# Kernel tuning notes

Hardware: AMD Instinct MI355X
Metric: run time of the kernel (lower is better)

## Reference

```python
import jax, jax.numpy as jnp
import numpy as np

B, S, H, E, R, V, NC = 256, 100, 512, 512, 50, 50000, 5


def setup_inputs() -> dict:
    key = jax.random.key(0)
    ks = jax.random.split(key, 16)
    g = lambda k, shp, s=0.05: jax.random.normal(k, shp, dtype=jnp.float32) * s
    return dict(
        sentence=jax.random.randint(ks[0], (B, S), 0, V),
        decoder_state=g(ks[1], (B, H), 1.0),
        encoder_outputs=g(ks[2], (B, S, H), 1.0),
        word_emb=g(ks[3], (V, E)),
        rel_emb=g(ks[4], (R + 1, E)),
        sos_emb=g(ks[5], (1, E)),
        W_comb=g(ks[6], (E, H + E)), b_comb=jnp.zeros((E,), jnp.float32),
        W_attn=g(ks[7], (1, 2 * H)), b_attn=jnp.zeros((1,), jnp.float32),
        W_ih=g(ks[8], (NC, 3 * H, E)), W_hh=g(ks[9], (NC, 3 * H, H)),
        b_ih=jnp.zeros((NC, 3 * H), jnp.float32), b_hh=jnp.zeros((NC, 3 * H), jnp.float32),
        W_eos=g(ks[10], (1, H)), b_eos=jnp.zeros((1,), jnp.float32),
        W_pred=g(ks[11], (R, H)), b_pred=jnp.zeros((R,), jnp.float32),
        W_fuse=g(ks[12], (100, 2 * H)), b_fuse=jnp.zeros((100,), jnp.float32),
        W_copy=g(ks[13], (1, 100)), b_copy=jnpp.zeros((1,), jnp.float32) if False else jnp.zeros((1,), jnp.float32),
    )


def _gru_step(x, h, Wih, Whh, bih, bhh):
    # torch GRU gate order: r, z, n
    gi = x @ Wih.T + bih          # [B, 3H]
    gh = h @ Whh.T + bhh          # [B, 3H]
    ir, iz, inn = jnp.split(gi, 3, axis=-1)
    hr, hz, hn = jnp.split(gh, 3, axis=-1)
    r = jax.nn.sigmoid(ir + hr)
    z = jax.nn.sigmoid(iz + hz)
    n = jnp.tanh(inn + r * hn)
    return (1.0 - z) * n + z * h


def _decode_step(emb, h, enc, cell, p):
    # attention: softmax over sequence dim of a 1-dim score
    h_exp = jnp.broadcast_to(h[:, None, :], enc.shape)          # [B, S, H]
    scores = jnp.concatenate([h_exp, enc], axis=-1) @ p['W_attn'].T + p['b_attn']  # [B,S,1]
    aw = jax.nn.softmax(scores, axis=1)
    context = jnp.sum(aw * enc, axis=1)                          # [B, H]
    x = jnp.concatenate([emb, context], axis=-1) @ p['W_comb'].T + p['b_comb']     # [B, E]
    h_new = _gru_step(x, h, p['W_ih'][cell], p['W_hh'][cell], p['b_ih'][cell], p['b_hh'][cell])
    out = h_new                                                  # GRU output == new state
    eos = out @ p['W_eos'].T + p['b_eos']                        # [B, 1]
    pred = jax.nn.log_softmax(jnp.concatenate([out @ p['W_pred'].T + p['b_pred'], eos], axis=-1), axis=-1)  # [B, R+1]
    fused = jax.nn.selu(jnp.concatenate([jnp.broadcast_to(out[:, None, :], enc.shape), enc], axis=-1))       # [B,S,2H]
    fused = jax.nn.selu(fused @ p['W_fuse'].T + p['b_fuse'])     # [B, S, 100]
    copy = (fused @ p['W_copy'].T + p['b_copy'])[..., 0]        # [B, S]
    copy = jax.nn.log_softmax(jnp.concatenate([copy, eos], axis=-1), axis=-1)  # [B, S+1]
    return pred, copy, h_new


def _forward(sentence, decoder_state, encoder_outputs, word_emb, rel_emb, sos_emb, p):
    b = sentence.shape[0]
    s = sentence.shape[1]
    output = jnp.broadcast_to(sos_emb[0], (b, sos_emb.shape[1]))  # SOS embedding
    enc_state = decoder_state
    prev_state = jnp.zeros_like(decoder_state)
    n_cells = p['W_ih'].shape[0]
    rel_logits, copy_logits, actions = [], [], []
    for c in range(n_cells):
        h = (enc_state + prev_state) * 0.5
        for t in range(3):
            pred, copy, h = _decode_step(output, h, encoder_outputs, c, p)
            if t == 0:
                act = jnp.argmax(pred, axis=1)                   # [B] in [0, R]
                rel_logits.append(pred)
                output = rel_emb[act]
            else:
                act = jnp.argmax(copy, axis=1)                   # [B] in [0, S]
                copy_logits.append(copy)
                word = jnp.take_along_axis(sentence, jnp.clip(act, 0, s - 1)[:, None], axis=1)[:, 0]
                output = word_emb[word]
            actions.append(act)
        prev_state = h
    return jnp.stack(rel_logits), jnp.stack(copy_logits), jnp.stack(actions)


def reference(sentence, decoder_state, encoder_outputs, word_emb, rel_emb, sos_emb,
              W_comb, b_comb, W_attn, b_attn, W_ih, W_hh, b_ih, b_hh,
              W_eos, b_eos, W_pred, b_pred, W_fuse, b_fuse, W_copy, b_copy):
    p = dict(W_comb=W_comb, b_comb=b_comb, W_attn=W_attn, b_attn=b_attn,
             W_ih=W_ih, W_hh=W_hh, b_ih=b_ih, b_hh=b_hh,
             W_eos=W_eos, b_eos=b_eos, W_pred=W_pred, b_pred=b_pred,
             W_fuse=W_fuse, b_fuse=b_fuse, W_copy=W_copy, b_copy=b_copy)
    return _forward(sentence, decoder_state, encoder_outputs, word_emb, rel_emb, sos_emb, p)
```

## Files before the change

kernel.cpp:

```cpp
#include <hip/hip_runtime.h>
#include <math.h>

#define B 256
#define S 100
#define H 512
#define E 512
#define R 50
#define NC 5
#define H3 1536

__device__ __forceinline__ float selu_f(float x){
    return x > 0.0f ? 1.0507009873554805f * x
                    : 1.7580993408473766f * expm1f(x);
}
__device__ __forceinline__ float wred_sum(float v){
    #pragma unroll
    for (int o = 32; o > 0; o >>= 1) v += __shfl_xor(v, o);
    return v;
}
__device__ __forceinline__ float wred_maxf(float v){
    #pragma unroll
    for (int o = 32; o > 0; o >>= 1) v = fmaxf(v, __shfl_xor(v, o));
    return v;
}

struct GSmem {
    alignas(16) float As[16][68];
    alignas(16) float Ws[16][132];
};

__device__ __forceinline__ void gemm64(
    GSmem& sm,
    const float* __restrict__ A, int lda, int M,
    const float* __restrict__ W, int ldw,
    const float* __restrict__ bias,
    const float* __restrict__ addm, int ldadd,
    float* __restrict__ C, int ldc,
    int N, int m0, int n0, int k0beg, int k0end, int seluA)
{
    const int t  = threadIdx.x;
    const int tx = t & 15;
    const int ty = t >> 4;
    const int lm = t >> 2,  lk  = (t & 3) << 2;
    const int lw = t >> 1,  lkw = (t & 1) << 3;
    int am = m0 + lm; if (am >= M) am = M - 1;
    const float* Ap = A + (size_t)am * lda + lk;
    const int nw = n0 + lw;
    const float* Wp = W + (size_t)nw * ldw + lkw;
    const bool wok = (nw < N);
    const float4 f40 = make_float4(0.f, 0.f, 0.f, 0.f);

    float4 ar = *(const float4*)(Ap + k0beg);
    if (seluA){ ar.x = selu_f(ar.x); ar.y = selu_f(ar.y); ar.z = selu_f(ar.z); ar.w = selu_f(ar.w); }
    float4 w0 = wok ? *(const float4*)(Wp + k0beg)     : f40;
    float4 w1 = wok ? *(const float4*)(Wp + k0beg + 4) : f40;

    float acc[4][8] = {};
    for (int k0 = k0beg; k0 < k0end; k0 += 16){
        if (k0 != k0beg) __syncthreads();
        sm.As[lk+0][lm] = ar.x; sm.As[lk+1][lm] = ar.y;
        sm.As[lk+2][lm] = ar.z; sm.As[lk+3][lm] = ar.w;
        sm.Ws[lkw+0][lw] = w0.x; sm.Ws[lkw+1][lw] = w0.y;
        sm.Ws[lkw+2][lw] = w0.z; sm.Ws[lkw+3][lw] = w0.w;
        sm.Ws[lkw+4][lw] = w1.x; sm.Ws[lkw+5][lw] = w1.y;
        sm.Ws[lkw+6][lw] = w1.z; sm.Ws[lkw+7][lw] = w1.w;
        __syncthreads();
        if (k0 + 16 < k0end){
            ar = *(const float4*)(Ap + k0 + 16);
            if (seluA){ ar.x = selu_f(ar.x); ar.y = selu_f(ar.y); ar.z = selu_f(ar.z); ar.w = selu_f(ar.w); }
            w0 = wok ? *(const float4*)(Wp + k0 + 16)     : f40;
            w1 = wok ? *(const float4*)(Wp + k0 + 16 + 4) : f40;
        }
        #pragma unroll
        for (int kk = 0; kk < 16; ++kk){
            const float4 av  = *(const float4*)&sm.As[kk][ty*4];
            const float4 wv0 = *(const float4*)&sm.Ws[kk][tx*4];
            const float4 wv1 = *(const float4*)&sm.Ws[kk][tx*4 + 64];
            const float aa[4] = {av.x, av.y, av.z, av.w};
            const float bb[8] = {wv0.x, wv0.y, wv0.z, wv0.w, wv1.x, wv1.y, wv1.z, wv1.w};
            #pragma unroll
            for (int i = 0; i < 4; ++i)
                #pragma unroll
                for (int j = 0; j < 8; ++j)
                    acc[i][j] += aa[i] * bb[j];
        }
    }
    #pragma unroll
    for (int i = 0; i < 4; ++i){
        const int m = m0 + ty*4 + i;
        if (m < M){
            #pragma unroll
            for (int j = 0; j < 8; ++j){
                const int n = n0 + ((j < 4) ? (tx*4 + j) : (64 + tx*4 + j - 4));
                if (n < N){
                    float vv = acc[i][j];
                    if (bias) vv += bias[n];
                    if (addm) vv += addm[(size_t)m * ldadd + n];
                    C[(size_t)m * ldc + n] = vv;
                }
            }
        }
    }
}

struct GS128 {
    alignas(16) float As[16][132];
    alignas(16) float Ws[16][132];
};

__device__ __forceinline__ void gemm128(
    GS128& sm,
    const float* __restrict__ A, int lda, int M,
    const float* __restrict__ W, int ldw,
    const float* __restrict__ bias,
    const float* __restrict__ addm, int ldadd,
    float* __restrict__ C, int ldc,
    int N, int m0, int n0, int K, int seluA)
{
    const int t  = threadIdx.x;
    const int tx = t & 15, ty = t >> 4;
    const int lr = t >> 1, lk = (t & 1) << 3;
    int am = m0 + lr; if (am >= M) am = M - 1;
    const float* Ap = A + (size_t)am * lda + lk;
    const int nw = n0 + lr;
    const float* Wp = W + (size_t)nw * ldw + lk;
    const bool wok = (nw < N);
    const float4 f40 = make_float4(0.f, 0.f, 0.f, 0.f);

    float4 a0 = *(const float4*)Ap;
    float4 a1 = *(const float4*)(Ap + 4);
    float4 w0 = wok ? *(const float4*)Wp       : f40;
    float4 w1 = wok ? *(const float4*)(Wp + 4) : f40;

    float acc[8][8] = {};
    for (int k0 = 0; k0 < K; k0 += 16){
        if (k0) __syncthreads();
        float4 sa0 = a0, sa1 = a1;
        if (seluA){
            sa0.x = selu_f(sa0.x); sa0.y = selu_f(sa0.y);
            sa0.z = selu_f(sa0.z); sa0.w = selu_f(sa0.w);
            sa1.x = selu_f(sa1.x); sa1.y = selu_f(sa1.y);
            sa1.z = selu_f(sa1.z); sa1.w = selu_f(sa1.w);
        }
        sm.As[lk+0][lr] = sa0.x; sm.As[lk+1][lr] = sa0.y;
        sm.As[lk+2][lr] = sa0.z; sm.As[lk+3][lr] = sa0.w;
        sm.As[lk+4][lr] = sa1.x; sm.As[lk+5][lr] = sa1.y;
        sm.As[lk+6][lr] = sa1.z; sm.As[lk+7][lr] = sa1.w;
        sm.Ws[lk+0][lr] = w0.x;  sm.Ws[lk+1][lr] = w0.y;
        sm.Ws[lk+2][lr] = w0.z;  sm.Ws[lk+3][lr] = w0.w;
        sm.Ws[lk+4][lr] = w1.x;  sm.Ws[lk+5][lr] = w1.y;
        sm.Ws[lk+6][lr] = w1.z;  sm.Ws[lk+7][lr] = w1.w;
        __syncthreads();
        if (k0 + 16 < K){
            a0 = *(const float4*)(Ap + k0 + 16);
            a1 = *(const float4*)(Ap + k0 + 20);
            w0 = wok ? *(const float4*)(Wp + k0 + 16) : f40;
            w1 = wok ? *(const float4*)(Wp + k0 + 20) : f40;
        }
        #pragma unroll
        for (int kk = 0; kk < 16; ++kk){
            const float4 av0 = *(const float4*)&sm.As[kk][ty*4];
            const float4 av1 = *(const float4*)&sm.As[kk][ty*4 + 64];
            const float4 wv0 = *(const float4*)&sm.Ws[kk][tx*4];
            const float4 wv1 = *(const float4*)&sm.Ws[kk][tx*4 + 64];
            const float aa[8] = {av0.x, av0.y, av0.z, av0.w, av1.x, av1.y, av1.z, av1.w};
            const float bb[8] = {wv0.x, wv0.y, wv0.z, wv0.w, wv1.x, wv1.y, wv1.z, wv1.w};
            #pragma unroll
            for (int i = 0; i < 8; ++i)
                #pragma unroll
                for (int j = 0; j < 8; ++j)
                    acc[i][j] += aa[i] * bb[j];
        }
    }
    #pragma unroll
    for (int i = 0; i < 8; ++i){
        const int m = m0 + ((i < 4) ? (ty*4 + i) : (64 + ty*4 + i - 4));
        if (m < M){
            #pragma unroll
            for (int j = 0; j < 8; ++j){
                const int n = n0 + ((j < 4) ? (tx*4 + j) : (64 + tx*4 + j - 4));
                if (n < N){
                    float vv = acc[i][j];
                    if (bias) vv += bias[n];
                    if (addm) vv += addm[(size_t)m * ldadd + n];
                    C[(size_t)m * ldc + n] = vv;
                }
            }
        }
    }
}

struct GemmJob {
    const float* A; int lda; long long sA; int M;
    const float* W; int ldw; long long sW;
    const float* bias; long long sBias;
    const float* addm; int ldadd; long long sAddm;
    float* C; int ldc; long long sC;
    int N, K, seluA;
    int nx, ny, base;
};
struct Jobs4 { GemmJob j[4]; };

__global__ __launch_bounds__(256) void k_mgemm(Jobs4 js)
{
    __shared__ GS128 sm;
    const int bid = blockIdx.x;
    GemmJob j;
    if      (bid >= js.j[3].base) j = js.j[3];
    else if (bid >= js.j[2].base) j = js.j[2];
    else if (bid >= js.j[1].base) j = js.j[1];
    else                          j = js.j[0];
    const int local = bid - j.base;
    const int z = local / (j.nx * j.ny);
    const int r = local % (j.nx * j.ny);
    const int y = r / j.nx, x = r % j.nx;
    gemm128(sm,
            j.A + (size_t)z * j.sA, j.lda, j.M,
            j.W + (size_t)z * j.sW, j.ldw,
            j.bias ? j.bias + (size_t)z * j.sBias : nullptr,
            j.addm ? j.addm + (size_t)z * j.sAddm : nullptr, j.ldadd,
            j.C + (size_t)z * j.sC, j.ldc,
            j.N, y * 128, x * 128, j.K, j.seluA);
}

__global__ __launch_bounds__(256) void k_pre0(
    const float* __restrict__ sos, const float* __restrict__ dec,
    const float* __restrict__ enc, const float* __restrict__ W_attn,
    const float* __restrict__ W_comb, const float* __restrict__ b_comb,
    const float* __restrict__ rel_emb, const float* __restrict__ W_fuse,
    float* __restrict__ emb, float* __restrict__ h0,
    float* __restrict__ WcT, float* __restrict__ xc,
    float* __restrict__ relx, float* __restrict__ v_buf)
{
    __shared__ __align__(16) char smraw[sizeof(GS128)];
    const int bid = blockIdx.x, t = threadIdx.x;
    if (bid < 8){
        for (int idx = bid * 256 + t; idx < B * E; idx += 8 * 256){
            emb[idx] = sos[idx & (E - 1)];
            h0[idx]  = 0.5f * dec[idx];
        }
    } else if (bid < 136){
        float (*tile)[65] = (float(*)[65])smraw;
        const int tt = bid - 8;
        const int bx = (tt & 15) * 64;
        const int by = (tt >> 4) * 64;
        const int c4 = (t & 15) * 4, rg = t >> 4;
        for (int rr = 0; rr < 64; rr += 16){
            float4 v = *(const float4*)(W_comb + (size_t)(by + rg + rr) * (H + E) + bx + c4);
            tile[rg + rr][c4+0] = v.x; tile[rg + rr][c4+1] = v.y;
            tile[rg + rr][c4+2] = v.z; tile[rg + rr][c4+3] = v.w;
        }
        __syncthreads();
        for (int rr = 0; rr < 64; rr += 16){
            WcT[(size_t)(bx + rg + rr) * E + by + c4 + 0] = tile[c4+0][rg + rr];
            WcT[(size_t)(bx + rg + rr) * E + by + c4 + 1] = tile[c4+1][rg + rr];
            WcT[(size_t)(bx + rg + rr) * E + by + c4 + 2] = tile[c4+2][rg + rr];
            WcT[(size_t)(bx + rg + rr) * E + by + c4 + 3] = tile[c4+3][rg + rr];
        }
    } else if (bid < 392){
        float* aw   = (float*)smraw;
        float* red  = aw + 128;
        float* ctxl = red + 128;
        const int b = bid - 136;
        const int wv = t >> 6, ln = t & 63;
        const float* eb = enc + (size_t)b * S * H;
        const float* wa = W_attn + H;
        for (int s = wv; s < S; s += 4){
            const float* es = eb + (size_t)s * H;
            float a = 0.f;
            #pragma unroll
            for (int u = 0; u < H/64; ++u) a += es[ln + 64*u] * wa[ln + 64*u];
            a = wred_sum(a);
            if (ln == 0) aw[s] = a;
        }
        __syncthreads();
        float vm = (t < S) ? aw[t] : -INFINITY;
        if (t < 128) red[t] = vm;
        __syncthreads();
        for (int st = 64; st > 0; st >>= 1){
            if (t < st) red[t] = fmaxf(red[t], red[t + st]);
            __syncthreads();
        }
        const float m = red[0];
        __syncthreads();
        float e = (t < S) ? expf(aw[t] - m) : 0.f;
        if (t < 128) red[t] = e;
        __syncthreads();
        for (int st = 64; st > 0; st >>= 1){
            if (t < st) red[t] += red[t + st];
            __syncthreads();
        }
        const float sum = red[0];
        __syncthreads();
        if (t < S) aw[t] = e / sum;
        __syncthreads();
        for (int hh = t; hh < H; hh += 256){
            float a = 0.f;
            for (int s = 0; s < S; ++s) a += aw[s] * eb[(size_t)s * H + hh];
            ctxl[hh] = a;
        }
        __syncthreads();
        for (int n = wv; n < E; n += 4){
            const float* wr = W_comb + (size_t)n * (H + E) + E;
            float a = 0.f;
            #pragma unroll
            for (int u = 0; u < H/64; ++u) a += ctxl[ln + 64*u] * wr[ln + 64*u];
            a = wred_sum(a);
            if (ln == 0) xc[(size_t)b * E + n] = a + b_comb[n];
        }
    } else if (bid < 396){
        GS128& sm = *(GS128*)smraw;
        gemm128(sm, rel_emb, E, R + 1, W_comb, H + E, nullptr, nullptr, 0,
                relx, E, E, 0, (bid - 392) * 128, E, 0);
    } else {
        GS128& sm = *(GS128*)smraw;
        gemm128(sm, enc, H, B * S, W_fuse + H, 2 * H, nullptr, nullptr, 0,
                v_buf, 100, 100, (bid - 396) * 128, 0, H, 1);
    }
}

struct GSmemK64 {
    alignas(16) float As[64][68];
    alignas(16) float Ws[64][132];
};

__global__ __launch_bounds__(256) void k_gru2_k64(
    const float* emb, const float* h,
    const float* Wihc, const float* Whh,
    const float* gixc, const float* bhh,
    float* gip, float* ghp, int giOn)
{
    __shared__ GSmemK64 sm;
    const int t = threadIdx.x;
    int xt = blockIdx.x;
    const int m0 = blockIdx.y * 64;
    const int z  = blockIdx.z;
    const int kb = z * 64;

    const float* A; int lda; const float* W; int ldw;
    const float* bias = nullptr; const float* addm = nullptr;
    float* C;
    if (giOn && xt < 12){
        A = emb; lda = E; W = Wihc; ldw = E;
        if (z == 0) addm = gixc;
        C = gip + (size_t)z * B * H3;
    } else {
        if (giOn) xt -= 12;
        A = h; lda = H; W = Whh; ldw = H;
        if (z == 0) bias = bhh;
        C = ghp + (size_t)z * B * H3;
    }
    const int n0 = xt * 128;

    {
        const int lm = t >> 2, ks = (t & 3) << 4;
        const float* Ap = A + (size_t)(m0 + lm) * lda + kb + ks;
        #pragma unroll
        for (int q = 0; q < 4; ++q){
            float4 a = *(const float4*)(Ap + 4*q);
            sm.As[ks + 4*q + 0][lm] = a.x;
            sm.As[ks + 4*q + 1][lm] = a.y;
            sm.As[ks + 4*q + 2][lm] = a.z;
            sm.As[ks + 4*q + 3][lm] = a.w;
        }
    }
    {
        const int lw = t >> 1, ks2 = (t & 1) << 5;
        const float* Wp = W + (size_t)(n0 + lw) * ldw + kb + ks2;
        #pragma unroll
        for (int q = 0; q < 8; ++q){
            float4 w = *(const float4*)(Wp + 4*q);
            sm.Ws[ks2 + 4*q + 0][lw] = w.x;
            sm.Ws[ks2 + 4*q + 1][lw] = w.y;
            sm.Ws[ks2 + 4*q + 2][lw] = w.z;
            sm.Ws[ks2 + 4*q + 3][lw] = w.w;
        }
    }
    __syncthreads();

    const int tx = t & 15, ty = t >> 4;
    float acc[4][8] = {};
    #pragma unroll 16
    for (int kk = 0; kk < 64; ++kk){
        const float4 av  = *(const float4*)&sm.As[kk][ty*4];
        const float4 wv0 = *(const float4*)&sm.Ws[kk][tx*4];
        const float4 wv1 = *(const float4*)&sm.Ws[kk][tx*4 + 64];
        const float aa[4] = {av.x, av.y, av.z, av.w};
        const float bb[8] = {wv0.x, wv0.y, wv0.z, wv0.w, wv1.x, wv1.y, wv1.z, wv1.w};
        #pragma unroll
        for (int i = 0; i < 4; ++i)
            #pragma unroll
            for (int j = 0; j < 8; ++j)
                acc[i][j] += aa[i] * bb[j];
    }
    #pragma unroll
    for (int i = 0; i < 4; ++i){
        const int m = m0 + ty*4 + i;
        #pragma unroll
        for (int j = 0; j < 8; ++j){
            const int n = n0 + ((j < 4) ? (tx*4 + j) : (64 + tx*4 + j - 4));
            float vv = acc[i][j];
            if (bias) vv += bias[n];
            if (addm) vv += addm[(size_t)m * H3 + n];
            C[(size_t)m * H3 + n] = vv;
        }
    }
}

__global__ __launch_bounds__(256) void k_gru2(
    const float* emb, const float* h,
    const float* Wihc, const float* Whh,
    const float* gixc, const float* bhh,
    float* gip, float* ghp, int giOn, int ksp)
{
    __shared__ GSmem sm;
    int xt = blockIdx.x;
    const int m0 = blockIdx.y * 64;
    const int z  = blockIdx.z;
    const int kt = H / ksp;
    const int kb = z * kt, ke = kb + kt;
    if (giOn && xt < 12){
        gemm64(sm, emb, E, B, Wihc, E, nullptr,
               (z == 0) ? gixc : nullptr, H3,
               gip + (size_t)z * B * H3, H3,
               H3, m0, xt * 128, kb, ke, 0);
    } else {
        if (giOn) xt -= 12;
        gemm64(sm, h, H, B, Whh, H,
               (z == 0) ? bhh : nullptr, nullptr, 0,
               ghp + (size_t)z * B * H3, H3,
               H3, m0, xt * 128, kb, ke, 0);
    }
}

__device__ __forceinline__ float gru_one(float gi_r, float gh_r, float gi_z, float gh_z,
                                         float gi_n, float gh_n, float hprev)
{
    const float r = 1.f / (1.f + expf(-(gi_r + gh_r)));
    const float z = 1.f / (1.f + expf(-(gi_z + gh_z)));
    const float n = tanhf(gi_n + r * gh_n);
    return (1.f - z) * n + z * hprev;
}

__global__ __launch_bounds__(256) void k_rel_fused(
    const float* __restrict__ gip, const float* __restrict__ ghp, int ksp,
    const float* __restrict__ hold,
    const float* __restrict__ Wp, const float* __restrict__ bp,
    const float* __restrict__ We, const float* __restrict__ be,
    const float* __restrict__ rel_gi_c,
    const float* __restrict__ gixc_c,
    float* __restrict__ gi_next,
    float* __restrict__ out_rel, int c,
    float* __restrict__ out_act,
    float* __restrict__ hnew_out)
{
    __shared__ alignas(16) float hn[H];
    __shared__ float logits[R + 1];
    __shared__ int   act_sh;
    const int b = blockIdx.x, t = threadIdx.x;
    const int wvi = t >> 6, ln = t & 63;
    const size_t gbase = (size_t)b * H3;
    {
        const int g = t << 1;
        float irx=0.f, iry=0.f, izx=0.f, izy=0.f, inx=0.f, iny=0.f;
        float hrx=0.f, hry=0.f, hzx=0.f, hzy=0.f, hnx=0.f, hny=0.f;
        for (int z = 0; z < ksp; ++z){
            const float* gp = gip + (size_t)z * B * H3 + gbase;
            const float* hp = ghp + (size_t)z * B * H3 + gbase;
            float2 v;
            v = *(const float2*)(gp + g);        irx += v.x; iry += v.y;
            v = *(const float2*)(gp + H + g);    izx += v.x; izy += v.y;
            v = *(const float2*)(gp + 2*H + g);  inx += v.x; iny += v.y;
            v = *(const float2*)(hp + g);        hrx += v.x; hry += v.y;
            v = *(const float2*)(hp + H + g);    hzx += v.x; hzy += v.y;
            v = *(const float2*)(hp + 2*H + g);  hnx += v.x; hny += v.y;
        }
        const float2 hprev = *(const float2*)(hold + (size_t)b * H + g);
        const float hv0 = gru_one(irx, hrx, izx, hzx, inx, hnx, hprev.x);
        const float hv1 = gru_one(iry, hry, izy, hzy, iny, hny, hprev.y);
        hn[g] = hv0; hn[g+1] = hv1;
        float2 hw; hw.x = hv0; hw.y = hv1;
        *(float2*)(hnew_out + (size_t)b * H + g) = hw;
    }
    __syncthreads();
    {
        const float4* hn4 = (const float4*)hn;
        const float4 h0 = hn4[ln*2], h1 = hn4[ln*2+1];
        for (int i = wvi; i < R + 1; i += 4){
            const float* wr = (i < R) ? Wp + (size_t)i * H : We;
            const float4* wr4 = (const float4*)wr;
            const float4 w0 = wr4[ln*2], w1 = wr4[ln*2+1];
            float a = h0.x*w0.x + h0.y*w0.y + h0.z*w0.z + h0.w*w0.w
                    + h1.x*w1.x + h1.y*w1.y + h1.z*w1.z + h1.w*w1.w;
            a = wred_sum(a);
            if (ln == 0) logits[i] = a + (i < R ? bp[i] : be[0]);
        }
    }
    __syncthreads();
    if (wvi == 0){
        const float v = (ln < R + 1) ? logits[ln] : -INFINITY;
        const float m = wred_maxf(v);
        const float p = v - m;
        const float e = (ln < R + 1) ? expf(p) : 0.f;
        const float lse = logf(wred_sum(e));
        const float q = p - lse;
        float bv = q; int bi = ln;
        #pragma unroll
        for (int o = 32; o > 0; o >>= 1){
            float ov = __shfl_xor(bv, o);
            int   oi = __shfl_xor(bi, o);
            if (ov > bv || (ov == bv && oi < bi)){ bv = ov; bi = oi; }
        }
        if (ln < R + 1)
            out_rel[(size_t)c * B * (R+1) + (size_t)b * (R+1) + ln] = q;
        if (ln == 0){
            out_act[(size_t)(3*c) * B + b] = (float)bi;
            act_sh = bi;
        }
    }
    __syncthreads();
    {
        const float4* rg4 = (const float4*)(rel_gi_c + (size_t)act_sh * H3);
        const float4* gx4 = (const float4*)(gixc_c + gbase);
        float4* go4 = (float4*)(gi_next + gbase);
        for (int u = t; u < H3/4; u += 256){
            float4 a = rg4[u], bq = gx4[u];
            a.x += bq.x; a.y += bq.y; a.z += bq.z; a.w += bq.w;
            go4[u] = a;
        }
    }
}

__global__ __launch_bounds__(256) void k_copy_fused(
    const float* __restrict__ gip, const float* __restrict__ ghp,
    int gi_full, int ksp,
    const float* __restrict__ hold,
    const float* __restrict__ v,
    const float* __restrict__ W_fuse, const float* __restrict__ b_fuse,
    const float* __restrict__ W_copy, const float* __restrict__ b_copy,
    const float* __restrict__ We, const float* __restrict__ be,
    const int* __restrict__ sentence, const float* __restrict__ word_emb,
    float* __restrict__ out_copy, int slot,
    float* __restrict__ emb, float* __restrict__ out_act, int aslot,
    float* __restrict__ hnew_out, const float* __restrict__ dec, int cell_end)
{
    __shared__ alignas(16) float hn[H];
    __shared__ alignas(16) float shl[H];
    __shared__ float u_lds[100];
    __shared__ float wc_lds[100];
    __shared__ float sco[101];
    __shared__ int   act_sh;
    const int b = blockIdx.x, t = threadIdx.x;
    const int wvi = t >> 6, ln = t & 63;
    const size_t gbase = (size_t)b * H3;
    {
        const int g = t << 1;
        float irx, iry, izx, izy, inx, iny;
        if (gi_full){
            float2 v2;
            v2 = *(const float2*)(gip + gbase + g);        irx = v2.x; iry = v2.y;
            v2 = *(const float2*)(gip + gbase + H + g);    izx = v2.x; izy = v2.y;
            v2 = *(const float2*)(gip + gbase + 2*H + g);  inx = v2.x; iny = v2.y;
        } else {
            irx = iry = izx = izy = inx = iny = 0.f;
            for (int z = 0; z < ksp; ++z){
                const float* gp = gip + (size_t)z * B * H3 + gbase;
                float2 v2;
                v2 = *(const float2*)(gp + g);        irx += v2.x; iry += v2.y;
                v2 = *(const float2*)(gp + H + g);    izx += v2.x; izy += v2.y;
                v2 = *(const float2*)(gp + 2*H + g);  inx += v2.x; iny += v2.y;
            }
        }
        float hrx=0.f, hry=0.f, hzx=0.f, hzy=0.f, hnx=0.f, hny=0.f;
        for (int z = 0; z < ksp; ++z){
            const float* hp = ghp + (size_t)z * B * H3 + gbase;
            float2 v2;
            v2 = *(const float2*)(hp + g);        hrx += v2.x; hry += v2.y;
            v2 = *(const float2*)(hp + H + g);    hzx += v2.x; hzy += v2.y;
            v2 = *(const float2*)(hp + 2*H + g);  hnx += v2.x; hny += v2.y;
        }
        const float2 hprev = *(const float2*)(hold + (size_t)b * H + g);
        const float hv0 = gru_one(irx, hrx, izx, hzx, inx, hnx, hprev.x);
        const float hv1 = gru_one(iry, hry, izy, hzy, iny, hny, hprev.y);
        hn[g] = hv0; hn[g+1] = hv1;
        shl[g] = selu_f(hv0); shl[g+1] = selu_f(hv1);
        float2 hw;
        if (cell_end){
            const float2 d2 = *(const float2*)(dec + (size_t)b * H + g);
            hw.x = 0.5f * (d2.x + hv0); hw.y = 0.5f * (d2.y + hv1);
        } else { hw.x = hv0; hw.y = hv1; }
        *(float2*)(hnew_out + (size_t)b * H + g) = hw;
    }
    if (t < 100) wc_lds[t] = W_copy[t];
    __syncthreads();
    {
        const float4* sh4 = (const float4*)shl;
        const float4 s0 = sh4[ln*2], s1 = sh4[ln*2+1];
        for (int n = wvi; n < 100; n += 4){
            const float4* wr4 = (const float4*)(W_fuse + (size_t)n * (2*H));
            const float4 w0 = wr4[ln*2], w1 = wr4[ln*2+1];
            float a = s0.x*w0.x + s0.y*w0.y + s0.z*w0.z + s0.w*w0.w
                    + s1.x*w1.x + s1.y*w1.y + s1.z*w1.z + s1.w*w1.w;
            a = wred_sum(a);
            if (ln == 0) u_lds[n] = a + b_fuse[n];
        }
        if (wvi == 3){
            const float4* hn4 = (const float4*)hn;
            const float4 h0 = hn4[ln*2], h1 = hn4[ln*2+1];
            const float4* we4 = (const float4*)We;
            const float4 w0 = we4[ln*2], w1 = we4[ln*2+1];
            float a = h0.x*w0.x + h0.y*w0.y + h0.z*w0.z + h0.w*w0.w
                    + h1.x*w1.x + h1.y*w1.y + h1.z*w1.z + h1.w*w1.w;
            a = wred_sum(a);
            if (ln == 0) sco[100] = a + be[0];
        }
    }
    __syncthreads();
    const float bc = b_copy[0];
    for (int s = wvi; s < S; s += 4){
        const float* vb = v + ((size_t)b * S + s) * 100;
        float a = selu_f(u_lds[ln] + vb[ln]) * wc_lds[ln];
        if (ln + 64 < 100) a += selu_f(u_lds[ln + 64] + vb[ln + 64]) * wc_lds[ln + 64];
        a = wred_sum(a);
        if (ln == 0) sco[s] = a + bc;
    }
    __syncthreads();
    if (wvi == 0){
        const float v1 = sco[ln];
        const int i2 = ln + 64;
        const float v2 = (i2 <= S) ? sco[i2] : -INFINITY;
        const float m = wred_maxf(fmaxf(v1, v2));
        const float p1 = v1 - m, p2 = v2 - m;
        float e = expf(p1) + ((i2 <= S) ? expf(p2) : 0.f);
        const float lse = logf(wred_sum(e));
        const float q1 = p1 - lse, q2 = p2 - lse;
        float bv; int bi;
        if (q2 > q1){ bv = q2; bi = i2; } else { bv = q1; bi = ln; }
        #pragma unroll
        for (int o = 32; o > 0; o >>= 1){
            float ov = __shfl_xor(bv, o);
            int   oi = __shfl_xor(bi, o);
            if (ov > bv || (ov == bv && oi < bi)){ bv = ov; bi = oi; }
        }
        const size_t obase = (size_t)slot * B * (S+1) + (size_t)b * (S+1);
        out_copy[obase + ln] = q1;
        if (i2 <= S) out_copy[obase + i2] = q2;
        if (ln == 0){
            out_act[(size_t)aslot * B + b] = (float)bi;
            act_sh = bi;
        }
    }
    __syncthreads();
    const int act = act_sh;
    const int wd = sentence[b * S + (act < S ? act : S - 1)];
    const float2* wr2 = (const float2*)(word_emb + (size_t)wd * E);
    ((float2*)(emb + (size_t)b * E))[t] = wr2[t];
}

extern "C" void kernel_launch(void* const* d_in, const int* in_sizes, int n_in,
                              void* d_out, int out_size, void* d_ws, size_t ws_size,
                              hipStream_t stream)
{
    (void)in_sizes; (void)n_in; (void)out_size;
    const int*   sentence = (const int*)  d_in[0];
    const float* dec      = (const float*)d_in[1];
    const float* enc      = (const float*)d_in[2];
    const float* word_emb = (const float*)d_in[3];
    const float* rel_emb  = (const float*)d_in[4];
    const float* sos      = (const float*)d_in[5];
    const float* W_comb   = (const float*)d_in[6];
    const float* b_comb   = (const float*)d_in[7];
    const float* W_attn   = (const float*)d_in[8];
    const float* W_ih     = (const float*)d_in[10];
    const float* W_hh     = (const float*)d_in[11];
    const float* b_ih     = (const float*)d_in[12];
    const float* b_hh     = (const float*)d_in[13];
    const float* W_eos    = (const float*)d_in[14];
    const float* b_eos    = (const float*)d_in[15];
    const float* W_pred   = (const float*)d_in[16];
    const float* b_pred   = (const float*)d_in[17];
    const float* W_fuse   = (const float*)d_in[18];
    const float* b_fuse   = (const float*)d_in[19];
    const float* W_copy   = (const float*)d_in[20];
    const float* b_copy   = (const float*)d_in[21];

    float* out       = (float*)d_out;
    float* out_rel   = out;
    float* out_copy  = out + (size_t)NC * B * (R + 1);
    float* out_act   = out_copy + (size_t)2 * NC * B * (S + 1);

    float* p = (float*)d_ws;
    float* v_buf  = p; p += (size_t)B * S * 100;
    float* Wihc   = p; p += (size_t)NC * H3 * E;
    float* gixc   = p; p += (size_t)NC * B * H3;
    float* rel_gi = p; p += (size_t)NC * 64 * H3;
    float* WcT    = p; p += (size_t)(H + E) * E;
    float* relx   = p; p += (size_t)64 * E;
    float* xc     = p; p += B * E;
    float* emb    = p; p += B * E;
    float* hb0    = p; p += B * H;
    float* hb1    = p; p += B * H;
    const size_t fixed_floats = (size_t)(p - (float*)d_ws);
    int ksp = 8;
    if ((fixed_floats + (size_t)2 * 8 * B * H3) * 4 > ws_size) ksp = 4;
    float* gip = p; p += (size_t)ksp * B * H3;
    float* ghp = p; p += (size_t)ksp * B * H3;
    float* hb[2] = { hb0, hb1 };

    k_pre0<<<596, 256, 0, stream>>>(sos, dec, enc, W_attn, W_comb, b_comb, rel_emb,
                                    W_fuse, emb, hb0, WcT, xc, relx, v_buf);

    Jobs4 js;
    js.j[0] = { W_ih, E, (long long)H3 * E, H3,
                WcT, E, 0, nullptr, 0, nullptr, 0, 0,
                Wihc, E, (long long)H3 * E, E, E, 0, 4, 12, 0 };
    js.j[1] = { xc, E, 0, B,
                W_ih, E, (long long)H3 * E, b_ih, H3, nullptr, 0, 0,
                gixc, H3, (long long)B * H3, H3, E, 0, 12, 2, 240 };
    js.j[2] = { relx, E, 0, R + 1,
                W_ih, E, (long long)H3 * E, nullptr, 0, nullptr, 0, 0,
                rel_gi, H3, (long long)64 * H3, H3, E, 0, 12, 1, 360 };
    js.j[3] = js.j[2];
    js.j[3].base = 1 << 30;
    k_mgemm<<<420, 256, 0, stream>>>(js);

    int cur = 0;
    for (int c = 0; c < NC; ++c){
        const float* Wihc_c = Wihc + (size_t)c * H3 * E;
        const float* Whh_c  = W_hh + (size_t)c * H3 * H;
        const float* gixc_c = gixc + (size_t)c * B * H3;
        const float* bhh_c  = b_hh + (size_t)c * H3;
        for (int t3 = 0; t3 < 3; ++t3){
            const int giOn = (t3 != 1);
            if (ksp == 8){
                k_gru2_k64<<<dim3(giOn ? 24 : 12, 4, 8), 256, 0, stream>>>(
                    emb, hb[cur], Wihc_c, Whh_c, gixc_c, bhh_c,
                    gip, ghp, giOn);
            } else {
                k_gru2<<<dim3(giOn ? 24 : 12, 4, ksp), 256, 0, stream>>>(
                    emb, hb[cur], Wihc_c, Whh_c, gixc_c, bhh_c,
                    gip, ghp, giOn, ksp);
            }
            if (t3 == 0){
                k_rel_fused<<<B, 256, 0, stream>>>(
                    gip, ghp, ksp, hb[cur], W_pred, b_pred, W_eos, b_eos,
                    rel_gi + (size_t)c * 64 * H3, gixc_c, gip,
                    out_rel, c, out_act, hb[cur^1]);
            } else {
                k_copy_fused<<<B, 256, 0, stream>>>(
                    gip, ghp, (t3 == 1) ? 1 : 0, ksp, hb[cur], v_buf,
                    W_fuse, b_fuse, W_copy, b_copy, W_eos, b_eos,
                    sentence, word_emb,
                    out_copy, 2*c + (t3-1), emb, out_act, 3*c + t3,
                    hb[cur^1], dec, (t3 == 2) ? 1 : 0);
            }
            cur ^= 1;
        }
    }
}
```

Measured before the change: 1.059 ms.

## Enlarge GRU split-K GEMM tile to 128x128 and move v_buf GEMM into mgemm

The per-step GRU gate GEMM now uses a 128x128 output tile (8x8 per thread) instead of 64x128, which halves the grid in M and doubles reuse of each loaded weight tile. The precompute of the encoder-fuse projection (v_buf) moves from k_pre0 into the multi-job GEMM launch as a fourth job, shrinking k_pre0. The larger tile raises LDS use and register pressure and halves the number of blocks per launch, which could lower occupancy. The pointer argument order of k_copy_fused is swapped together with its call site.

```diff
diff --git a/kernel.cpp b/kernel.cpp
--- a/kernel.cpp
+++ b/kernel.cpp
@@ -227,10 +227,10 @@
     const float* __restrict__ sos, const float* __restrict__ dec,
     const float* __restrict__ enc, const float* __restrict__ W_attn,
     const float* __restrict__ W_comb, const float* __restrict__ b_comb,
-    const float* __restrict__ rel_emb, const float* __restrict__ W_fuse,
+    const float* __restrict__ rel_emb,
     float* __restrict__ emb, float* __restrict__ h0,
     float* __restrict__ WcT, float* __restrict__ xc,
-    float* __restrict__ relx, float* __restrict__ v_buf)
+    float* __restrict__ relx)
 {
     __shared__ __align__(16) char smraw[sizeof(GS128)];
     const int bid = blockIdx.x, t = threadIdx.x;
@@ -308,32 +308,28 @@
             a = wred_sum(a);
             if (ln == 0) xc[(size_t)b * E + n] = a + b_comb[n];
         }
-    } else if (bid < 396){
+    } else {
         GS128& sm = *(GS128*)smraw;
         gemm128(sm, rel_emb, E, R + 1, W_comb, H + E, nullptr, nullptr, 0,
                 relx, E, E, 0, (bid - 392) * 128, E, 0);
-    } else {
-        GS128& sm = *(GS128*)smraw;
-        gemm128(sm, enc, H, B * S, W_fuse + H, 2 * H, nullptr, nullptr, 0,
-                v_buf, 100, 100, (bid - 396) * 128, 0, H, 1);
-    }
-}
-
-struct GSmemK64 {
-    alignas(16) float As[64][68];
+    }
+}
+
+struct GSK128 {
+    alignas(16) float As[64][132];
     alignas(16) float Ws[64][132];
 };
 
-__global__ __launch_bounds__(256) void k_gru2_k64(
+__global__ __launch_bounds__(256) void k_gru2_k128(
     const float* emb, const float* h,
     const float* Wihc, const float* Whh,
     const float* gixc, const float* bhh,
     float* gip, float* ghp, int giOn)
 {
-    __shared__ GSmemK64 sm;
+    __shared__ GSK128 sm;
     const int t = threadIdx.x;
     int xt = blockIdx.x;
-    const int m0 = blockIdx.y * 64;
+    const int m0 = blockIdx.y * 128;
     const int z  = blockIdx.z;
     const int kb = z * 64;
 
@@ -353,49 +349,47 @@
     const int n0 = xt * 128;
 
     {
-        const int lm = t >> 2, ks = (t & 3) << 4;
-        const float* Ap = A + (size_t)(m0 + lm) * lda + kb + ks;
+        const int lr = t >> 1, lk = (t & 1) << 5;
+        const float* Ap = A + (size_t)(m0 + lr) * lda + kb + lk;
         #pragma unroll
-        for (int q = 0; q < 4; ++q){
+        for (int q = 0; q < 8; ++q){
             float4 a = *(const float4*)(Ap + 4*q);
-            sm.As[ks + 4*q + 0][lm] = a.x;
-            sm.As[ks + 4*q + 1][lm] = a.y;
-            sm.As[ks + 4*q + 2][lm] = a.z;
-            sm.As[ks + 4*q + 3][lm] = a.w;
-        }
-    }
-    {
-        const int lw = t >> 1, ks2 = (t & 1) << 5;
-        const float* Wp = W + (size_t)(n0 + lw) * ldw + kb + ks2;
+            sm.As[lk + 4*q + 0][lr] = a.x;
+            sm.As[lk + 4*q + 1][lr] = a.y;
+            sm.As[lk + 4*q + 2][lr] = a.z;
+            sm.As[lk + 4*q + 3][lr] = a.w;
+        }
+        const float* Wp = W + (size_t)(n0 + lr) * ldw + kb + lk;
         #pragma unroll
         for (int q = 0; q < 8; ++q){
             float4 w = *(const float4*)(Wp + 4*q);
-            sm.Ws[ks2 + 4*q + 0][lw] = w.x;
-            sm.Ws[ks2 + 4*q + 1][lw] = w.y;
-            sm.Ws[ks2 + 4*q + 2][lw] = w.z;
-            sm.Ws[ks2 + 4*q + 3][lw] = w.w;
+            sm.Ws[lk + 4*q + 0][lr] = w.x;
+            sm.Ws[lk + 4*q + 1][lr] = w.y;
+            sm.Ws[lk + 4*q + 2][lr] = w.z;
+            sm.Ws[lk + 4*q + 3][lr] = w.w;
         }
     }
     __syncthreads();
 
     const int tx = t & 15, ty = t >> 4;
-    float acc[4][8] = {};
-    #pragma unroll 16
+    float acc[8][8] = {};
+    #pragma unroll 8
     for (int kk = 0; kk < 64; ++kk){
-        const float4 av  = *(const float4*)&sm.As[kk][ty*4];
+        const float4 av0 = *(const float4*)&sm.As[kk][ty*4];
+        const float4 av1 = *(const float4*)&sm.As[kk][ty*4 + 64];
         const float4 wv0 = *(const float4*)&sm.Ws[kk][tx*4];
         const float4 wv1 = *(const float4*)&sm.Ws[kk][tx*4 + 64];
-        const float aa[4] = {av.x, av.y, av.z, av.w};
+        const float aa[8] = {av0.x, av0.y, av0.z, av0.w, av1.x, av1.y, av1.z, av1.w};
         const float bb[8] = {wv0.x, wv0.y, wv0.z, wv0.w, wv1.x, wv1.y, wv1.z, wv1.w};
         #pragma unroll
-        for (int i = 0; i < 4; ++i)
+        for (int i = 0; i < 8; ++i)
             #pragma unroll
             for (int j = 0; j < 8; ++j)
                 acc[i][j] += aa[i] * bb[j];
     }
     #pragma unroll
-    for (int i = 0; i < 4; ++i){
-        const int m = m0 + ty*4 + i;
+    for (int i = 0; i < 8; ++i){
+        const int m = m0 + ((i < 4) ? (ty*4 + i) : (64 + ty*4 + i - 4));
         #pragma unroll
         for (int j = 0; j < 8; ++j){
             const int n = n0 + ((j < 4) ? (tx*4 + j) : (64 + tx*4 + j - 4));
@@ -534,8 +528,8 @@
 __global__ __launch_bounds__(256) void k_copy_fused(
     const float* __restrict__ gip, const float* __restrict__ ghp,
     int gi_full, int ksp,
+    const float* __restrict__ v,
     const float* __restrict__ hold,
-    const float* __restrict__ v,
     const float* __restrict__ W_fuse, const float* __restrict__ b_fuse,
     const float* __restrict__ W_copy, const float* __restrict__ b_copy,
     const float* __restrict__ We, const float* __restrict__ be,
@@ -707,8 +701,8 @@
     float* ghp = p; p += (size_t)ksp * B * H3;
     float* hb[2] = { hb0, hb1 };
 
-    k_pre0<<<596, 256, 0, stream>>>(sos, dec, enc, W_attn, W_comb, b_comb, rel_emb,
-                                    W_fuse, emb, hb0, WcT, xc, relx, v_buf);
+    k_pre0<<<396, 256, 0, stream>>>(sos, dec, enc, W_attn, W_comb, b_comb, rel_emb,
+                                    emb, hb0, WcT, xc, relx);
 
     Jobs4 js;
     js.j[0] = { W_ih, E, (long long)H3 * E, H3,
@@ -720,9 +714,10 @@
     js.j[2] = { relx, E, 0, R + 1,
                 W_ih, E, (long long)H3 * E, nullptr, 0, nullptr, 0, 0,
                 rel_gi, H3, (long long)64 * H3, H3, E, 0, 12, 1, 360 };
-    js.j[3] = js.j[2];
-    js.j[3].base = 1 << 30;
-    k_mgemm<<<420, 256, 0, stream>>>(js);
+    js.j[3] = { enc, H, 0, B * S,
+                W_fuse + H, 2 * H, 0, nullptr, 0, nullptr, 0, 0,
+                v_buf, 100, 0, 100, H, 1, 1, 200, 420 };
+    k_mgemm<<<620, 256, 0, stream>>>(js);
 
     int cur = 0;
     for (int c = 0; c < NC; ++c){
@@ -733,7 +728,7 @@
         for (int t3 = 0; t3 < 3; ++t3){
             const int giOn = (t3 != 1);
             if (ksp == 8){
-                k_gru2_k64<<<dim3(giOn ? 24 : 12, 4, 8), 256, 0, stream>>>(
+                k_gru2_k128<<<dim3(giOn ? 24 : 12, 2, 8), 256, 0, stream>>>(
                     emb, hb[cur], Wihc_c, Whh_c, gixc_c, bhh_c,
                     gip, ghp, giOn);
             } else {
@@ -748,7 +743,7 @@
                     out_rel, c, out_act, hb[cur^1]);
             } else {
                 k_copy_fused<<<B, 256, 0, stream>>>(
-                    gip, ghp, (t3 == 1) ? 1 : 0, ksp, hb[cur], v_buf,
+                    gip, ghp, (t3 == 1) ? 1 : 0, ksp, v_buf, hb[cur],
                     W_fuse, b_fuse, W_copy, b_copy, W_eos, b_eos,
                     sentence, word_emb,
                     out_copy, 2*c + (t3-1), emb, out_act, 3*c + t3,
```

New measurement: 1.291 ms. 21.9% more time.
